# Optimization experiments

Hardware: AMD Instinct MI355X
Metric: run time of the kernel (lower is better)

The kernel has to match this reference:

```python
import jax, jax.numpy as jnp
import numpy as np

N_NODES = 20000   # len(set(idx_i)); edge targets cover all nodes
N_EDGES = 320000
F = 128           # feature dim f
N_RBF = 20        # n radial basis functions
R_CUT = 5.0


def setup_inputs() -> dict:
    key = jax.random.key(0)
    ks = jax.random.split(key, 8)
    s = jax.random.normal(ks[0], (N_EDGES, 1, F), dtype=jnp.float32)
    r = jax.random.normal(ks[1], (N_EDGES, 3), dtype=jnp.float32)
    v = jax.random.normal(ks[2], (N_EDGES, 3, F), dtype=jnp.float32)
    idx_i = jax.random.randint(ks[3], (N_EDGES,), 0, N_NODES, dtype=jnp.int32)
    W_phi = jax.random.normal(ks[4], (F, 3 * F), dtype=jnp.float32) * 0.05
    b_phi = jnp.zeros((3 * F,), dtype=jnp.float32)
    W_w = jax.random.normal(ks[5], (N_RBF, 3 * F), dtype=jnp.float32) * 0.05
    b_w = jnp.zeros((3 * F,), dtype=jnp.float32)
    return {"s": s, "r": r, "v": v, "idx_i": idx_i,
            "W_phi": W_phi, "b_phi": b_phi, "W_w": W_w, "b_w": b_w}


def reference(s, r, v, idx_i, W_phi, b_phi, W_w, b_w):
    # phi network: [E,1,F] -> [E,1,3F]
    phi_out = jnp.einsum('eif,fg->eig', s, W_phi) + b_phi

    # RBF on edge vector norms: [E,1,1] -> [E,1,n]
    r_norm = jnp.linalg.norm(r, axis=1, keepdims=True)[:, :, None]  # [E,1,1]
    n_vals = jnp.arange(1, N_RBF + 1, dtype=jnp.float32)            # [n]
    rbf = jnp.sin(n_vals * (jnp.pi / R_CUT) * r_norm) / r_norm      # [E,1,n]
    # cosine cutoff applied to rbf values (faithful to source)
    rbf = jnp.where(rbf <= R_CUT,
                    0.5 * (jnp.cos(jnp.pi * rbf / R_CUT) + 1.0),
                    jnp.zeros_like(rbf))

    # w network: [E,1,n] -> [E,1,3F]
    w = jnp.einsum('ein,ng->eig', rbf, W_w) + b_w

    split = w * phi_out                    # [E,1,3F]
    sp0 = split[..., :F]                   # gates v
    sp1 = split[..., F:2 * F]              # scalar message
    sp2 = split[..., 2 * F:]               # gates direction

    # scatter-add scalar messages -> [N,1,F]
    out_s = jax.ops.segment_sum(sp1, idx_i, num_segments=N_NODES)

    # direction term: detached r, normalized by GLOBAL Frobenius norm (faithful)
    org_r = jax.lax.stop_gradient(r)
    org_r = org_r / jnp.linalg.norm(org_r)         # [E,3]
    dir_msg = sp2 * org_r[:, :, None]              # [E,3,F]
    v_msg = dir_msg + sp0 * v                      # [E,3,F]

    # scatter-add vector messages -> [N,3,F]
    out_v = jax.ops.segment_sum(v_msg, idx_i, num_segments=N_NODES)
    return out_v, out_s
```

## Files before the change

kernel.cpp:

```cpp
#include <hip/hip_runtime.h>
#include <hip/hip_bf16.h>
#include <math.h>

#define E_TOT   320000
#define NNODE   20000
#define FDIM    128
#define N3F     384
#define NRBF    20
#define OV_SIZE (NNODE * 3 * FDIM)
#define DMAX    16

typedef __attribute__((ext_vector_type(8))) short short8;
typedef __attribute__((ext_vector_type(4))) short short4v;
typedef __attribute__((ext_vector_type(4))) float f32x4;

__device__ __forceinline__ short f2bf(float x) {
  union { float f; unsigned u; } v; v.f = x;
  unsigned r = (v.u + 0x7fffu + ((v.u >> 16) & 1u)) >> 16;
  return (short)r;
}

__global__ void sumsq_kernel(const float* __restrict__ r, float* __restrict__ ws, int n) {
  int tid = blockIdx.x * blockDim.x + threadIdx.x;
  float acc = 0.f;
  for (int i = tid; i < n; i += gridDim.x * blockDim.x) {
    float x = r[i];
    acc += x * x;
  }
  for (int off = 32; off > 0; off >>= 1) acc += __shfl_down(acc, off);
  __shared__ float s[4];
  int lane = threadIdx.x & 63, w = threadIdx.x >> 6;
  if (lane == 0) s[w] = acc;
  __syncthreads();
  if (threadIdx.x == 0) {
    float t = s[0] + s[1] + s[2] + s[3];
    unsafeAtomicAdd(ws, t);
  }
}

__global__ void prep_kernel(const float* __restrict__ Wphi, const float* __restrict__ Ww,
                            short* __restrict__ frag) {
  int g = blockIdx.x * 256 + threadIdx.x;
  int lane = g & 63;
  int fid  = g >> 6;
  short* out = frag + (size_t)g * 8;
  if (fid < 96) {
    int ntile = fid >> 2, ks = fid & 3;
    int n  = ntile * 16 + (lane & 15);
    int kb = ks * 32 + (lane >> 4) * 8;
#pragma unroll
    for (int j = 0; j < 8; ++j) out[j] = f2bf(Wphi[(kb + j) * N3F + n]);
  } else if (fid < 120) {
    int ntile = fid - 96;
    int n  = ntile * 16 + (lane & 15);
    int kb = (lane >> 4) * 8;
#pragma unroll
    for (int j = 0; j < 8; ++j) {
      int k = kb + j;
      out[j] = (k < NRBF) ? f2bf(Ww[k * N3F + n]) : (short)0;
    }
  }
}

__global__ void hist_kernel(const int* __restrict__ idx, int* __restrict__ cnt) {
  int e = blockIdx.x * 256 + threadIdx.x;
  if (e < E_TOT) atomicAdd(&cnt[idx[e]], 1);
}

__global__ void scan_kernel(const int* __restrict__ cnt, int* __restrict__ cursor) {
  __shared__ int part[256];
  __shared__ int base_sh[256];
  const int t = threadIdx.x;
  int lo = t * 79; if (lo > NNODE) lo = NNODE;
  int hi = t * 79 + 79; if (hi > NNODE) hi = NNODE;
  int s = 0;
  for (int i = lo; i < hi; ++i) s += cnt[i];
  part[t] = s;
  __syncthreads();
  if (t == 0) {
    int run = 0;
    for (int i = 0; i < 256; ++i) { base_sh[i] = run; run += part[i]; }
  }
  __syncthreads();
  int run = base_sh[t];
  for (int i = lo; i < hi; ++i) { cursor[i] = run; run += cnt[i]; }
}

__global__ void scatter_kernel(const int* __restrict__ idx, int* __restrict__ cursor,
                               int* __restrict__ perm) {
  int e = blockIdx.x * 256 + threadIdx.x;
  if (e < E_TOT) {
    int p = atomicAdd(&cursor[idx[e]], 1);
    perm[p] = e;
  }
}

template <bool USE_PERM>
__launch_bounds__(256, 4)
__global__ void main_kernel(const float* __restrict__ s_in, const float* __restrict__ r_in,
                            const float* __restrict__ v_in, const int* __restrict__ idx_in,
                            const float* __restrict__ bphi_in, const float* __restrict__ bw_in,
                            const short* __restrict__ frag, const float* __restrict__ ws_sumsq,
                            const int* __restrict__ perm, float* __restrict__ out) {
  __shared__ __align__(16) char pool[DMAX * 512 * 4];
  short* sh_s   = (short*)pool;
  short* sh_rbf = (short*)(pool + 64 * 136 * 2);
  float* acc    = (float*)pool;
  __shared__ float sh_bphi[N3F];
  __shared__ float sh_bw[N3F];
  __shared__ float sh_orgr[64][4];
  __shared__ int   sh_perm[64];
  __shared__ int   sh_lid[64];
  __shared__ int   sh_nodes[64];
  __shared__ int   sh_d;

  const int tid = threadIdx.x;
  const int e0  = blockIdx.x * 64;
  const float inv_gnorm = 1.0f / sqrtf(ws_sumsq[0]);

  if (tid < 64) {
    int pe = USE_PERM ? perm[e0 + tid] : (e0 + tid);
    sh_perm[tid] = pe;
    int node = idx_in[pe];
    float rx = r_in[pe * 3 + 0], ry = r_in[pe * 3 + 1], rz = r_in[pe * 3 + 2];
    float rn = sqrtf(rx * rx + ry * ry + rz * rz);
    float irn = 1.0f / rn;
    sh_orgr[tid][0] = rx * inv_gnorm;
    sh_orgr[tid][1] = ry * inv_gnorm;
    sh_orgr[tid][2] = rz * inv_gnorm;
    const float c0 = 0.62831853071795864769f;
#pragma unroll
    for (int n = 1; n <= NRBF; ++n) {
      float t = sinf(((float)n * c0) * rn) * irn;
      float val = (t <= 5.0f) ? 0.5f * (cosf(c0 * t) + 1.0f) : 0.0f;
      sh_rbf[tid * 40 + (n - 1)] = f2bf(val);
    }
#pragma unroll
    for (int k = NRBF; k < 32; ++k) sh_rbf[tid * 40 + k] = 0;
    int prev = __shfl_up(node, 1);
    int flag = (tid == 0) || (node != prev);
    unsigned long long m = __ballot(flag);
    int lid = (int)__popcll(m & ((2ull << tid) - 1ull)) - 1;
    sh_lid[tid] = lid;
    if (flag) sh_nodes[lid] = node;
    if (tid == 0) sh_d = (int)__popcll(m);
  }
  for (int j = tid; j < N3F; j += 256) {
    sh_bphi[j] = bphi_in[j];
    sh_bw[j]   = bw_in[j];
  }
  __syncthreads();

#pragma unroll
  for (int it = 0; it < 8; ++it) {
    int idx4 = tid + it * 256;
    int row = idx4 >> 5, kq = idx4 & 31;
    const float4* srow = (const float4*)(s_in + (size_t)sh_perm[row] * FDIM);
    float4 val = srow[kq];
    short4v p = { f2bf(val.x), f2bf(val.y), f2bf(val.z), f2bf(val.w) };
    *(short4v*)&sh_s[row * 136 + kq * 4] = p;
  }
  __syncthreads();

  const int wave = tid >> 6, lane = tid & 63;
  const int col  = lane & 15;
  const int q    = lane >> 4;

  const int arow = wave * 16 + col;
  short8 a_phi[4];
#pragma unroll
  for (int ks = 0; ks < 4; ++ks)
    a_phi[ks] = *(const short8*)&sh_s[arow * 136 + ks * 32 + q * 8];
  short8 a_w = *(const short8*)&sh_rbf[arow * 40 + q * 8];

  int   lid4[4]; int vbase[4];
  float orx[4], ory[4], orz[4];
#pragma unroll
  for (int i = 0; i < 4; ++i) {
    int el = wave * 16 + q * 4 + i;
    lid4[i]  = sh_lid[el];
    vbase[i] = sh_perm[el] * (3 * FDIM);
    orx[i] = sh_orgr[el][0];
    ory[i] = sh_orgr[el][1];
    orz[i] = sh_orgr[el][2];
  }
  const int d = sh_d;
  const bool use_lds = USE_PERM && (d <= DMAX);

  __syncthreads();
  if (use_lds) {
    for (int j = tid; j < (d << 9); j += 256) acc[j] = 0.f;
  }
  __syncthreads();

  float* out_v = out;
  float* out_s = out + OV_SIZE;
  const short8* fp = (const short8*)frag;
  const short8* fw = fp + 96 * 64;

  for (int f = 0; f < 8; ++f) {
    const int nt0 = f, nt1 = f + 8, nt2 = f + 16;
    f32x4 accP0 = {0.f, 0.f, 0.f, 0.f}, accP1 = accP0, accP2 = accP0;
    f32x4 accW0 = accP0, accW1 = accP0, accW2 = accP0;
#pragma unroll
    for (int ks = 0; ks < 4; ++ks) {
      short8 b0 = fp[(nt0 * 4 + ks) * 64 + lane];
      short8 b1 = fp[(nt1 * 4 + ks) * 64 + lane];
      short8 b2 = fp[(nt2 * 4 + ks) * 64 + lane];
      accP0 = __builtin_amdgcn_mfma_f32_16x16x32_bf16(a_phi[ks], b0, accP0, 0, 0, 0);
      accP1 = __builtin_amdgcn_mfma_f32_16x16x32_bf16(a_phi[ks], b1, accP1, 0, 0, 0);
      accP2 = __builtin_amdgcn_mfma_f32_16x16x32_bf16(a_phi[ks], b2, accP2, 0, 0, 0);
    }
    accW0 = __builtin_amdgcn_mfma_f32_16x16x32_bf16(a_w, fw[nt0 * 64 + lane], accW0, 0, 0, 0);
    accW1 = __builtin_amdgcn_mfma_f32_16x16x32_bf16(a_w, fw[nt1 * 64 + lane], accW1, 0, 0, 0);
    accW2 = __builtin_amdgcn_mfma_f32_16x16x32_bf16(a_w, fw[nt2 * 64 + lane], accW2, 0, 0, 0);

    const int feat = f * 16 + col;
    const float bp0 = sh_bphi[feat], bp1 = sh_bphi[feat + 128], bp2 = sh_bphi[feat + 256];
    const float bw0 = sh_bw[feat],   bw1 = sh_bw[feat + 128],   bw2 = sh_bw[feat + 256];

    auto flush = [&](int l, float as, float avx, float avy, float avz) {
      if (use_lds) {
        atomicAdd(&acc[(l << 9) + feat], as);
        atomicAdd(&acc[(l << 9) + 128 + feat], avx);
        atomicAdd(&acc[(l << 9) + 256 + feat], avy);
        atomicAdd(&acc[(l << 9) + 384 + feat], avz);
      } else {
        int node = sh_nodes[l];
        unsafeAtomicAdd(&out_s[node * FDIM + feat], as);
        unsafeAtomicAdd(&out_v[(node * 3 + 0) * FDIM + feat], avx);
        unsafeAtomicAdd(&out_v[(node * 3 + 1) * FDIM + feat], avy);
        unsafeAtomicAdd(&out_v[(node * 3 + 2) * FDIM + feat], avz);
      }
    };

    float as = 0.f, avx = 0.f, avy = 0.f, avz = 0.f;
    int cur = lid4[0];
#pragma unroll
    for (int i = 0; i < 4; ++i) {
      float sp0 = (accW0[i] + bw0) * (accP0[i] + bp0);
      float sp1 = (accW1[i] + bw1) * (accP1[i] + bp1);
      float sp2 = (accW2[i] + bw2) * (accP2[i] + bp2);
      const float* vp = v_in + (size_t)vbase[i] + feat;
      float mx = sp2 * orx[i] + sp0 * vp[0];
      float my = sp2 * ory[i] + sp0 * vp[FDIM];
      float mz = sp2 * orz[i] + sp0 * vp[2 * FDIM];
      if (lid4[i] != cur) {
        flush(cur, as, avx, avy, avz);
        as = avx = avy = avz = 0.f;
        cur = lid4[i];
      }
      as += sp1; avx += mx; avy += my; avz += mz;
    }
    flush(cur, as, avx, avy, avz);
  }

  if (use_lds) {
    __syncthreads();
    for (int j = tid; j < (d << 9); j += 256) {
      int l = j >> 9, rem = j & 511, comp = rem >> 7, ft = rem & 127;
      int node = sh_nodes[l];
      float val = acc[j];
      float* dst = (comp == 0) ? &out_s[node * FDIM + ft]
                               : &out_v[(node * 3 + (comp - 1)) * FDIM + ft];
      if (l > 0 && l < d - 1) *dst = val;
      else unsafeAtomicAdd(dst, val);
    }
  }
}

extern "C" void kernel_launch(void* const* d_in, const int* in_sizes, int n_in,
                              void* d_out, int out_size, void* d_ws, size_t ws_size,
                              hipStream_t stream) {
  const float* s_in  = (const float*)d_in[0];
  const float* r_in  = (const float*)d_in[1];
  const float* v_in  = (const float*)d_in[2];
  const int*   idx_i = (const int*)d_in[3];
  const float* Wphi  = (const float*)d_in[4];
  const float* bphi  = (const float*)d_in[5];
  const float* Ww    = (const float*)d_in[6];
  const float* bw    = (const float*)d_in[7];
  float* out = (float*)d_out;

  const size_t WS_NEED_SORTED = 1562896;
  const bool use_sorted = (ws_size >= WS_NEED_SORTED);

  float* ws_sumsq = (float*)d_ws;
  int*   cnt      = (int*)((char*)d_ws + 16);
  short* frag_s   = (short*)((char*)d_ws + 80016);
  int*   cursor   = (int*)((char*)d_ws + 202896);
  int*   permv    = (int*)((char*)d_ws + 282896);
  short* frag_f   = (short*)((char*)d_ws + 16);
  short* frag     = use_sorted ? frag_s : frag_f;

  hipMemsetAsync(d_out, 0, (size_t)out_size * sizeof(float), stream);
  hipMemsetAsync(d_ws, 0, use_sorted ? 80016 : 16, stream);
  sumsq_kernel<<<480, 256, 0, stream>>>(r_in, ws_sumsq, in_sizes[1]);
  prep_kernel<<<30, 256, 0, stream>>>(Wphi, Ww, frag);
  if (use_sorted) {
    hist_kernel<<<1250, 256, 0, stream>>>(idx_i, cnt);
    scan_kernel<<<1, 256, 0, stream>>>(cnt, cursor);
    scatter_kernel<<<1250, 256, 0, stream>>>(idx_i, cursor, permv);
    main_kernel<true><<<E_TOT / 64, 256, 0, stream>>>(s_in, r_in, v_in, idx_i, bphi, bw,
                                                      frag, ws_sumsq, permv, out);
  } else {
    main_kernel<false><<<E_TOT / 64, 256, 0, stream>>>(s_in, r_in, v_in, idx_i, bphi, bw,
                                                       frag, ws_sumsq, nullptr, out);
  }
}
```

Baseline: 989.8 us.

## Split RBF work across waves, prefetch v before MFMA, tune occupancy and DMAX

The RBF computation is spread over all four waves instead of one, and uses fast __sinf/__cosf intrinsics. Each feature iteration now loads its v values into registers before the MFMA block so those loads overlap the matrix math, and it adds a __syncthreads at the top of the iteration. DMAX drops from 16 to 12, which shrinks the LDS pool, and the launch bounds change to an amdgpu_waves_per_eu(4,5) hint. The costs are an extra barrier every iteration, reduced accuracy from the fast trig, and more blocks taking the global-atomic path.

```diff
diff --git a/kernel.cpp b/kernel.cpp
--- a/kernel.cpp
+++ b/kernel.cpp
@@ -8,7 +8,7 @@
 #define N3F     384
 #define NRBF    20
 #define OV_SIZE (NNODE * 3 * FDIM)
-#define DMAX    16
+#define DMAX    12
 
 typedef __attribute__((ext_vector_type(8))) short short8;
 typedef __attribute__((ext_vector_type(4))) short short4v;
@@ -96,7 +96,8 @@
 }
 
 template <bool USE_PERM>
-__launch_bounds__(256, 4)
+__attribute__((amdgpu_waves_per_eu(4, 5)))
+__launch_bounds__(256)
 __global__ void main_kernel(const float* __restrict__ s_in, const float* __restrict__ r_in,
                             const float* __restrict__ v_in, const int* __restrict__ idx_in,
                             const float* __restrict__ bphi_in, const float* __restrict__ bw_in,
@@ -118,32 +119,36 @@
   const int e0  = blockIdx.x * 64;
   const float inv_gnorm = 1.0f / sqrtf(ws_sumsq[0]);
 
-  if (tid < 64) {
-    int pe = USE_PERM ? perm[e0 + tid] : (e0 + tid);
-    sh_perm[tid] = pe;
-    int node = idx_in[pe];
+  {
+    const int er = tid & 63, part = tid >> 6;
+    int pe = USE_PERM ? perm[e0 + er] : (e0 + er);
     float rx = r_in[pe * 3 + 0], ry = r_in[pe * 3 + 1], rz = r_in[pe * 3 + 2];
     float rn = sqrtf(rx * rx + ry * ry + rz * rz);
     float irn = 1.0f / rn;
-    sh_orgr[tid][0] = rx * inv_gnorm;
-    sh_orgr[tid][1] = ry * inv_gnorm;
-    sh_orgr[tid][2] = rz * inv_gnorm;
     const float c0 = 0.62831853071795864769f;
-#pragma unroll
-    for (int n = 1; n <= NRBF; ++n) {
-      float t = sinf(((float)n * c0) * rn) * irn;
-      float val = (t <= 5.0f) ? 0.5f * (cosf(c0 * t) + 1.0f) : 0.0f;
-      sh_rbf[tid * 40 + (n - 1)] = f2bf(val);
-    }
-#pragma unroll
-    for (int k = NRBF; k < 32; ++k) sh_rbf[tid * 40 + k] = 0;
-    int prev = __shfl_up(node, 1);
-    int flag = (tid == 0) || (node != prev);
-    unsigned long long m = __ballot(flag);
-    int lid = (int)__popcll(m & ((2ull << tid) - 1ull)) - 1;
-    sh_lid[tid] = lid;
-    if (flag) sh_nodes[lid] = node;
-    if (tid == 0) sh_d = (int)__popcll(m);
+    if (part == 0) {
+      sh_perm[er] = pe;
+      int node = idx_in[pe];
+      sh_orgr[er][0] = rx * inv_gnorm;
+      sh_orgr[er][1] = ry * inv_gnorm;
+      sh_orgr[er][2] = rz * inv_gnorm;
+#pragma unroll
+      for (int k = NRBF; k < 32; ++k) sh_rbf[er * 40 + k] = 0;
+      int prev = __shfl_up(node, 1);
+      int flag = (er == 0) || (node != prev);
+      unsigned long long m = __ballot(flag);
+      int lid = (int)__popcll(m & ((2ull << er) - 1ull)) - 1;
+      sh_lid[er] = lid;
+      if (flag) sh_nodes[lid] = node;
+      if (er == 0) sh_d = (int)__popcll(m);
+    }
+#pragma unroll
+    for (int j = 0; j < 5; ++j) {
+      int n = part * 5 + j + 1;
+      float t = __sinf(((float)n * c0) * rn) * irn;
+      float val = (t <= 5.0f) ? 0.5f * (__cosf(c0 * t) + 1.0f) : 0.0f;
+      sh_rbf[er * 40 + (n - 1)] = f2bf(val);
+    }
   }
   for (int j = tid; j < N3F; j += 256) {
     sh_bphi[j] = bphi_in[j];
@@ -173,13 +178,14 @@
     a_phi[ks] = *(const short8*)&sh_s[arow * 136 + ks * 32 + q * 8];
   short8 a_w = *(const short8*)&sh_rbf[arow * 40 + q * 8];
 
-  int   lid4[4]; int vbase[4];
+  int   lid4[4];
+  const float* vrow[4];
   float orx[4], ory[4], orz[4];
 #pragma unroll
   for (int i = 0; i < 4; ++i) {
     int el = wave * 16 + q * 4 + i;
-    lid4[i]  = sh_lid[el];
-    vbase[i] = sh_perm[el] * (3 * FDIM);
+    lid4[i] = sh_lid[el];
+    vrow[i] = v_in + (size_t)sh_perm[el] * (3 * FDIM);
     orx[i] = sh_orgr[el][0];
     ory[i] = sh_orgr[el][1];
     orz[i] = sh_orgr[el][2];
@@ -199,6 +205,18 @@
   const short8* fw = fp + 96 * 64;
 
   for (int f = 0; f < 8; ++f) {
+    __syncthreads();
+
+    const int feat = f * 16 + col;
+
+    float vx[4], vy[4], vz[4];
+#pragma unroll
+    for (int i = 0; i < 4; ++i) {
+      vx[i] = vrow[i][feat];
+      vy[i] = vrow[i][feat + FDIM];
+      vz[i] = vrow[i][feat + 2 * FDIM];
+    }
+
     const int nt0 = f, nt1 = f + 8, nt2 = f + 16;
     f32x4 accP0 = {0.f, 0.f, 0.f, 0.f}, accP1 = accP0, accP2 = accP0;
     f32x4 accW0 = accP0, accW1 = accP0, accW2 = accP0;
@@ -215,7 +233,6 @@
     accW1 = __builtin_amdgcn_mfma_f32_16x16x32_bf16(a_w, fw[nt1 * 64 + lane], accW1, 0, 0, 0);
     accW2 = __builtin_amdgcn_mfma_f32_16x16x32_bf16(a_w, fw[nt2 * 64 + lane], accW2, 0, 0, 0);
 
-    const int feat = f * 16 + col;
     const float bp0 = sh_bphi[feat], bp1 = sh_bphi[feat + 128], bp2 = sh_bphi[feat + 256];
     const float bw0 = sh_bw[feat],   bw1 = sh_bw[feat + 128],   bw2 = sh_bw[feat + 256];
 
@@ -241,10 +258,9 @@
       float sp0 = (accW0[i] + bw0) * (accP0[i] + bp0);
       float sp1 = (accW1[i] + bw1) * (accP1[i] + bp1);
       float sp2 = (accW2[i] + bw2) * (accP2[i] + bp2);
-      const float* vp = v_in + (size_t)vbase[i] + feat;
-      float mx = sp2 * orx[i] + sp0 * vp[0];
-      float my = sp2 * ory[i] + sp0 * vp[FDIM];
-      float mz = sp2 * orz[i] + sp0 * vp[2 * FDIM];
+      float mx = sp2 * orx[i] + sp0 * vx[i];
+      float my = sp2 * ory[i] + sp0 * vy[i];
+      float mz = sp2 * orz[i] + sp0 * vz[i];
       if (lid4[i] != cur) {
         flush(cur, as, avx, avy, avz);
         as = avx = avy = avz = 0.f;
```

Result: no change. 979.3 us (-1.1%).
